# Kernel optimization log

Hardware: AMD Instinct MI355X
Metric: run time of the kernel (lower is better)

The kernel has to match this reference:

```python
import jax, jax.numpy as jnp
import numpy as np

N = 100000
E = 600000
H = 128
G = 64          # number of graphs
LN_EPS = 1e-5


def setup_inputs() -> dict:
    key = jax.random.key(0)
    ks = jax.random.split(key, 16)
    node = jax.random.normal(ks[0], (N, H), dtype=jnp.float32)
    edge_index = jax.random.randint(ks[1], (2, E), 0, N, dtype=jnp.int64)
    edge_attr = jax.random.normal(ks[2], (E, 1), dtype=jnp.float32)
    batch_ptr = jnp.sort(jax.random.randint(ks[3], (N,), 0, G, dtype=jnp.int64))
    s = 1.0 / np.sqrt(H)
    params = dict(
        eps=jnp.float32(0.0),  # GINConv train_eps=True, init 0
        W1=jax.random.uniform(ks[4], (H, H), jnp.float32, -s, s),
        b1=jnp.zeros((H,), jnp.float32),
        g1=jnp.ones((H,), jnp.float32), be1=jnp.zeros((H,), jnp.float32),
        W2=jax.random.uniform(ks[5], (H, H), jnp.float32, -s, s),
        b2=jnp.zeros((H,), jnp.float32),
        g2=jnp.ones((H,), jnp.float32), be2=jnp.zeros((H,), jnp.float32),
        W3=jax.random.uniform(ks[6], (H, H), jnp.float32, -s, s),
        b3=jnp.zeros((H,), jnp.float32),
        ln_w=jnp.ones((H,), jnp.float32), ln_b=jnp.zeros((H,), jnp.float32),
    )
    return dict(node=node, edge_index=edge_index, edge_attr=edge_attr,
                batch_ptr=batch_ptr, **params)


def _layernorm(x, g, b):
    mu = x.mean(-1, keepdims=True)
    var = ((x - mu) ** 2).mean(-1, keepdims=True)
    return (x - mu) * jax.lax.rsqrt(var + LN_EPS) * g + b


def _forward(node, edge_index, batch_ptr, eps, W1, b1, g1, be1, W2, b2, g2, be2,
             W3, b3, ln_w, ln_b):
    src, dst = edge_index[0], edge_index[1]
    # GIN sum aggregation: scatter-add neighbor features to targets
    agg = jax.ops.segment_sum(node[src], dst, num_segments=N)  # [N, H]
    h = (1.0 + eps) * node + agg
    # 3-layer MLP (PyG MLP: lin -> LayerNorm -> ReLU, final lin plain)
    h = jax.nn.relu(_layernorm(h @ W1 + b1, g1, be1))
    h = jax.nn.relu(_layernorm(h @ W2 + b2, g2, be2))
    h = h @ W3 + b3
    # PyG graph-mode LayerNorm: normalize over all nodes+features per graph
    cnt = jax.ops.segment_sum(jnp.ones((N,), h.dtype), batch_ptr, num_segments=G)
    norm = jnp.maximum(cnt * H, 1.0)                       # [G]
    mean = jax.ops.segment_sum(h.sum(-1), batch_ptr, num_segments=G) / norm
    hc = h - mean[batch_ptr][:, None]
    var = jax.ops.segment_sum((hc * hc).sum(-1), batch_ptr, num_segments=G) / norm
    out = hc * jax.lax.rsqrt(var + LN_EPS)[batch_ptr][:, None] * ln_w + ln_b
    return jax.nn.relu(out)


def reference(node, edge_index, edge_attr, batch_ptr, eps, W1, b1, g1, be1,
              W2, b2, g2, be2, W3, b3, ln_w, ln_b):
    del edge_attr  # accepted by GIN_Layer.forward but unused
    return _forward(node, edge_index, batch_ptr, eps, W1, b1, g1, be1,
                    W2, b2, g2, be2, W3, b3, ln_w, ln_b)
```

## Files before the change

### kernel.cpp

```cpp
#include <hip/hip_runtime.h>

#define N_NODES 100000
#define N_EDGES 600000
#define H 128
#define G_NUM 64
#define LN_EPS 1e-5f

#define WSTR 136

#define NTILES ((N_NODES + 63) / 64)

#define SCAN_CHUNK 1024
#define SCAN_NB ((N_NODES + SCAN_CHUNK - 1) / SCAN_CHUNK)
#define HIST_NB ((N_EDGES + 255) / 256)
#define CVT_NB ((N_NODES * H / 8 + 255) / 256)
#define FILL_NB ((N_EDGES + 255) / 256)
#define WT_NB ((3 * 16384 + 255) / 256)

#define SCR_MAX 272

#define WT_IOFF   900612
#define NBF_IOFF  925192
#define H0_BF_IOFF (NBF_IOFF + N_NODES * (H / 2))
#define NEEDED_MIN ((size_t)(NBF_IOFF + N_NODES * (H / 2)) * 4)
#define NEEDED_BF  ((size_t)(H0_BF_IOFF + N_NODES * (H / 2)) * 4)

typedef __attribute__((ext_vector_type(8))) short short8;
typedef __attribute__((ext_vector_type(4))) float floatx4;

__device__ __forceinline__ unsigned short f2bf(float x) {
    unsigned int u = __float_as_uint(x);
    u += 0x7fffu + ((u >> 16) & 1u);
    return (unsigned short)(u >> 16);
}

__global__ __launch_bounds__(256) void hist_cvt_kernel(
    const int* __restrict__ ei, int* __restrict__ deg,
    const float* __restrict__ node, unsigned int* __restrict__ node_bf)
{
    int gb = blockIdx.x;
    if (gb < HIST_NB) {
        int e = gb * 256 + threadIdx.x;
        if (e >= N_EDGES) return;
        atomicAdd(&deg[ei[N_EDGES + e]], 1);
    } else {
        int i = (gb - HIST_NB) * 256 + threadIdx.x;
        if (i >= N_NODES * H / 8) return;
        float4 a = ((const float4*)node)[i * 2];
        float4 b = ((const float4*)node)[i * 2 + 1];
        uint4 p;
        p.x = (unsigned)f2bf(a.x) | ((unsigned)f2bf(a.y) << 16);
        p.y = (unsigned)f2bf(a.z) | ((unsigned)f2bf(a.w) << 16);
        p.z = (unsigned)f2bf(b.x) | ((unsigned)f2bf(b.y) << 16);
        p.w = (unsigned)f2bf(b.z) | ((unsigned)f2bf(b.w) << 16);
        ((uint4*)node_bf)[i] = p;
    }
}

__global__ __launch_bounds__(256) void scan1_kernel(
    const int* __restrict__ deg, int* __restrict__ off,
    int* __restrict__ blksum)
{
    __shared__ int sA[256], sB[256];
    const int tid = threadIdx.x;
    const int base = blockIdx.x * SCAN_CHUNK + tid * 4;
    int v[4];
#pragma unroll
    for (int j = 0; j < 4; ++j) {
        int i = base + j;
        v[j] = (i < N_NODES) ? deg[i] : 0;
    }
    int tsum = v[0] + v[1] + v[2] + v[3];
    int* a = sA; int* b = sB;
    a[tid] = tsum;
    __syncthreads();
#pragma unroll
    for (int o = 1; o < 256; o <<= 1) {
        int t = a[tid] + ((tid >= o) ? a[tid - o] : 0);
        b[tid] = t;
        __syncthreads();
        int* tmp = a; a = b; b = tmp;
    }
    int run = a[tid] - tsum;
#pragma unroll
    for (int j = 0; j < 4; ++j) {
        int i = base + j;
        if (i < N_NODES) off[i] = run;
        run += v[j];
    }
    if (tid == 255) blksum[blockIdx.x] = a[255];
}

__global__ __launch_bounds__(256) void scan23_kernel(
    int* __restrict__ off, const int* __restrict__ blksum,
    int* __restrict__ cursor)
{
    __shared__ int sA[128], sB[128];
    const int tid = threadIdx.x;
    if (tid < 128) sA[tid] = (tid < SCAN_NB) ? blksum[tid] : 0;
    __syncthreads();
    int* a = sA; int* b = sB;
#pragma unroll
    for (int o = 1; o < 128; o <<= 1) {
        int t = 0;
        if (tid < 128) t = a[tid] + ((tid >= o) ? a[tid - o] : 0);
        __syncthreads();
        if (tid < 128) b[tid] = t;
        __syncthreads();
        int* tmp = a; a = b; b = tmp;
    }
    int excl = 0;
    if (tid < 128) excl = a[tid] - ((tid < SCAN_NB) ? blksum[tid] : 0);
    __syncthreads();
    if (tid < 128) sA[tid] = excl;
    __syncthreads();

    int i = blockIdx.x * 256 + tid;
    if (i < N_NODES) {
        int val = off[i] + sA[i >> 10];
        off[i] = val;
        cursor[i] = val;
    }
    if (i == 0) off[N_NODES] = N_EDGES;
}

__global__ __launch_bounds__(256) void fill_wt_kernel(
    const int* __restrict__ ei, int* __restrict__ cursor,
    int* __restrict__ csr,
    const float* __restrict__ W1, const float* __restrict__ W2,
    const float* __restrict__ W3, unsigned short* __restrict__ WT)
{
    int gb = blockIdx.x;
    if (gb < FILL_NB) {
        int e = gb * 256 + threadIdx.x;
        if (e >= N_EDGES) return;
        int dst = ei[N_EDGES + e];
        int pos = atomicAdd(&cursor[dst], 1);
        csr[pos] = ei[e];
    } else {
        int idx = (gb - FILL_NB) * 256 + threadIdx.x;
        if (idx >= 3 * 16384) return;
        int l = idx >> 14, r = idx & 16383;
        int frag = r >> 3, j = r & 7;
        int lane = frag & 63, ktnt = frag >> 6;
        int kt = ktnt & 3, nt = ktnt >> 2;
        int c = lane & 15, q = lane >> 4;
        int n = nt * 16 + c;
        int k = kt * 32 + q * 8 + j;
        const float* W = (l == 0) ? W1 : ((l == 1) ? W2 : W3);
        WT[l * 16384 + r] = f2bf(W[k * 128 + n]);
    }
}

template <bool NBF>
__global__ __launch_bounds__(256) void gather_kernel(
    const float* __restrict__ node, const unsigned int* __restrict__ nbf,
    const int* __restrict__ off, const int* __restrict__ csr,
    const float* __restrict__ epsp, unsigned int* __restrict__ h0)
{
    __shared__ int scr4[4][SCR_MAX];
    const int tid = threadIdx.x;
    const int w = tid >> 6, lane = tid & 63;
    const int n0 = blockIdx.x * 64 + w * 16;

    const float2* np2 = (const float2*)node;
    const float epsv = 1.0f + epsp[0];

    auto ld = [&](int n) -> float2 {
        if constexpr (NBF) {
            unsigned int u = nbf[(size_t)n * 64 + lane];
            return make_float2(__uint_as_float(u << 16),
                               __uint_as_float(u & 0xffff0000u));
        } else {
            return np2[(size_t)n * 64 + lane];
        }
    };

    int oidx = n0 + ((lane < 17) ? lane : 16);
    if (oidx > N_NODES) oidx = N_NODES;
    const int offl = off[oidx];
    const int e_begin = __shfl(offl, 0);
    const int e_end   = __shfl(offl, 16);
    const int cnt = e_end - e_begin;

    int* scr = scr4[w];

    if (cnt <= SCR_MAX) {
        for (int k = lane; k < cnt; k += 64) scr[k] = csr[e_begin + k];
        __threadfence_block();

#pragma unroll
        for (int g4 = 0; g4 < 4; ++g4) {
            int p[4], e[4];
#pragma unroll
            for (int j = 0; j < 4; ++j) {
                p[j] = __shfl(offl, g4 * 4 + j) - e_begin;
                e[j] = __shfl(offl, g4 * 4 + j + 1) - e_begin;
            }
            float2 acc[4];
#pragma unroll
            for (int j = 0; j < 4; ++j) {
                int n = n0 + g4 * 4 + j;
                if (n < N_NODES) {
                    float2 own = ld(n);
                    acc[j] = make_float2(epsv * own.x, epsv * own.y);
                } else {
                    acc[j] = make_float2(0.f, 0.f);
                }
            }
            bool a0[4], a1[4];
            float2 b0[4], b1[4];
#pragma unroll
            for (int j = 0; j < 4; ++j) {
                a0[j] = p[j] < e[j];
                b0[j] = make_float2(0.f, 0.f);
                if (a0[j]) {
                    int nb = __builtin_amdgcn_readfirstlane(scr[p[j]]);
                    b0[j] = ld(nb);
                }
            }
#pragma unroll
            for (int j = 0; j < 4; ++j) {
                a1[j] = (p[j] + 1) < e[j];
                b1[j] = make_float2(0.f, 0.f);
                if (a1[j]) {
                    int nb = __builtin_amdgcn_readfirstlane(scr[p[j] + 1]);
                    b1[j] = ld(nb);
                }
            }
            while (a0[0] || a0[1] || a0[2] || a0[3]) {
                float2 b2[4]; bool a2[4];
#pragma unroll
                for (int j = 0; j < 4; ++j) {
                    a2[j] = (p[j] + 2) < e[j];
                    b2[j] = make_float2(0.f, 0.f);
                    if (a2[j]) {
                        int nb = __builtin_amdgcn_readfirstlane(scr[p[j] + 2]);
                        b2[j] = ld(nb);
                    }
                }
#pragma unroll
                for (int j = 0; j < 4; ++j) {
                    if (a0[j]) {
                        acc[j].x += b0[j].x; acc[j].y += b0[j].y;
                        p[j] += 1;
                    }
                    a0[j] = a1[j]; b0[j] = b1[j];
                    a1[j] = a2[j]; b1[j] = b2[j];
                }
            }
#pragma unroll
            for (int j = 0; j < 4; ++j) {
                int n = n0 + g4 * 4 + j;
                if (n < N_NODES) {
                    unsigned int pk = (unsigned)f2bf(acc[j].x) |
                                      ((unsigned)f2bf(acc[j].y) << 16);
                    h0[(size_t)n * 64 + lane] = pk;
                }
            }
        }
    } else {
#pragma unroll
        for (int g4 = 0; g4 < 4; ++g4) {
            float2 acc[4];
#pragma unroll
            for (int j = 0; j < 4; ++j) {
                int n = n0 + g4 * 4 + j;
                if (n < N_NODES) {
                    float2 own = ld(n);
                    acc[j] = make_float2(epsv * own.x, epsv * own.y);
                } else {
                    acc[j] = make_float2(0.f, 0.f);
                }
            }
            for (int j = 0; j < 4; ++j) {
                int n = n0 + g4 * 4 + j;
                if (n >= N_NODES) continue;
                for (int t = off[n]; t < off[n + 1]; ++t) {
                    float2 v = ld(csr[t]);
                    acc[j].x += v.x; acc[j].y += v.y;
                }
            }
#pragma unroll
            for (int j = 0; j < 4; ++j) {
                int n = n0 + g4 * 4 + j;
                if (n < N_NODES) {
                    unsigned int pk = (unsigned)f2bf(acc[j].x) |
                                      ((unsigned)f2bf(acc[j].y) << 16);
                    h0[(size_t)n * 64 + lane] = pk;
                }
            }
        }
    }
}

__device__ __forceinline__ void gemm_frags(const unsigned short* hIn,
                                           const unsigned short* __restrict__ WTl,
                                           floatx4 acc[8], int w, int lane)
{
    const int c = lane & 15, q = lane >> 4;
#pragma unroll
    for (int nt = 0; nt < 8; ++nt) acc[nt] = (floatx4){0.f, 0.f, 0.f, 0.f};
#pragma unroll
    for (int kt = 0; kt < 4; ++kt) {
        short8 a = *(const short8*)&hIn[(w * 16 + c) * WSTR + kt * 32 + q * 8];
#pragma unroll
        for (int nt = 0; nt < 8; ++nt) {
            short8 b = *(const short8*)&WTl[(nt * 256 + kt * 64 + lane) * 8];
            acc[nt] = __builtin_amdgcn_mfma_f32_16x16x32_bf16(a, b, acc[nt], 0, 0, 0);
        }
    }
}

__device__ __forceinline__ void gemm_layer_ln(unsigned short* h,
                                              const unsigned short* __restrict__ WTl,
                                              const float* __restrict__ bias,
                                              const float* __restrict__ g,
                                              const float* __restrict__ be,
                                              int w, int lane)
{
    const int c = lane & 15, q = lane >> 4;
    floatx4 acc[8];
    gemm_frags(h, WTl, acc, w, lane);

    float sum[4] = {0.f, 0.f, 0.f, 0.f};
    float sq[4]  = {0.f, 0.f, 0.f, 0.f};
#pragma unroll
    for (int nt = 0; nt < 8; ++nt) {
        float bv = bias[nt * 16 + c];
#pragma unroll
        for (int i = 0; i < 4; ++i) {
            float vv = acc[nt][i] + bv;
            acc[nt][i] = vv;
            sum[i] += vv; sq[i] += vv * vv;
        }
    }
#pragma unroll
    for (int m = 1; m < 16; m <<= 1) {
#pragma unroll
        for (int i = 0; i < 4; ++i) {
            sum[i] += __shfl_xor(sum[i], m);
            sq[i]  += __shfl_xor(sq[i], m);
        }
    }
    float mu[4], rstd[4];
#pragma unroll
    for (int i = 0; i < 4; ++i) {
        mu[i]   = sum[i] * (1.0f / 128.0f);
        rstd[i] = rsqrtf(sq[i] * (1.0f / 128.0f) - mu[i] * mu[i] + LN_EPS);
    }
#pragma unroll
    for (int nt = 0; nt < 8; ++nt) {
        float gw = g[nt * 16 + c];
        float bw = be[nt * 16 + c];
#pragma unroll
        for (int i = 0; i < 4; ++i) {
            float val = fmaxf(0.f, (acc[nt][i] - mu[i]) * rstd[i] * gw + bw);
            h[(w * 16 + q * 4 + i) * WSTR + nt * 16 + c] = f2bf(val);
        }
    }
}

__global__ __launch_bounds__(256) void mlp_kernel(
    const unsigned int* __restrict__ h0,
    const unsigned short* __restrict__ WT,
    const float* __restrict__ b1, const float* __restrict__ g1,
    const float* __restrict__ be1,
    const float* __restrict__ b2, const float* __restrict__ g2,
    const float* __restrict__ be2,
    const float* __restrict__ b3, const int* __restrict__ batch,
    float* __restrict__ out, float* __restrict__ gstat)
{
    __shared__ unsigned short hA[64 * WSTR];
    __shared__ float prm[7 * 128];
    __shared__ float s_gsum[G_NUM], s_gsq[G_NUM], s_gcnt[G_NUM];

    const int tid = threadIdx.x;
    const int w = tid >> 6, lane = tid & 63;
    const int row0 = blockIdx.x * 64;

    if (tid < G_NUM) { s_gsum[tid] = 0.f; s_gsq[tid] = 0.f; s_gcnt[tid] = 0.f; }
    {
        const float* srcs[7] = {b1, g1, be1, b2, g2, be2, b3};
#pragma unroll
        for (int t = 0; t < 4; ++t) {
            int i = tid + t * 256;
            if (i < 7 * 128) prm[i] = srcs[i >> 7][i & 127];
        }
    }

    {
        const int r = tid >> 2;
        const int q4 = tid & 3;
        uint4* d = (uint4*)(((unsigned int*)hA) + r * (WSTR / 2) + q4 * 16);
        const int row = row0 + r;
        if (row < N_NODES) {
            const uint4* s = (const uint4*)&h0[(size_t)row * 64 + q4 * 16];
#pragma unroll
            for (int k = 0; k < 4; ++k) d[k] = s[k];
        } else {
            uint4 z = make_uint4(0, 0, 0, 0);
#pragma unroll
            for (int k = 0; k < 4; ++k) d[k] = z;
        }
    }
    __syncthreads();

    gemm_layer_ln(hA, WT,         &prm[0],   &prm[128], &prm[256], w, lane);
    gemm_layer_ln(hA, WT + 16384, &prm[384], &prm[512], &prm[640], w, lane);

    {
        const int c = lane & 15, q = lane >> 4;
        floatx4 acc3[8];
        gemm_frags(hA, WT + 32768, acc3, w, lane);
        float sum[4] = {0.f, 0.f, 0.f, 0.f};
        float sq[4]  = {0.f, 0.f, 0.f, 0.f};
#pragma unroll
        for (int nt = 0; nt < 8; ++nt) {
            float bv = prm[768 + nt * 16 + c];
#pragma unroll
            for (int i = 0; i < 4; ++i) {
                float vv = acc3[nt][i] + bv;
                size_t nrow = (size_t)row0 + w * 16 + q * 4 + i;
                if (nrow < N_NODES)
                    out[nrow * H + nt * 16 + c] = vv;
                sum[i] += vv; sq[i] += vv * vv;
            }
        }
#pragma unroll
        for (int m = 1; m < 16; m <<= 1) {
#pragma unroll
            for (int i = 0; i < 4; ++i) {
                sum[i] += __shfl_xor(sum[i], m);
                sq[i]  += __shfl_xor(sq[i], m);
            }
        }
        if (c == 0) {
#pragma unroll
            for (int i = 0; i < 4; ++i) {
                size_t nrow = (size_t)row0 + w * 16 + q * 4 + i;
                if (nrow < N_NODES) {
                    int g = batch[nrow];
                    atomicAdd(&s_gsum[g], sum[i]);
                    atomicAdd(&s_gsq[g], sq[i]);
                    atomicAdd(&s_gcnt[g], 1.0f);
                }
            }
        }
    }
    __syncthreads();
    if (tid < G_NUM && s_gcnt[tid] > 0.f) {
        unsafeAtomicAdd(&gstat[tid], s_gsum[tid]);
        unsafeAtomicAdd(&gstat[G_NUM + tid], s_gsq[tid]);
        unsafeAtomicAdd(&gstat[2 * G_NUM + tid], s_gcnt[tid]);
    }
}

__global__ __launch_bounds__(256) void final_ln_kernel(
    float* __restrict__ h3, const int* __restrict__ batch,
    const float* __restrict__ lnw, const float* __restrict__ lnb,
    const float* __restrict__ gstat)
{
    int idx4 = blockIdx.x * 256 + threadIdx.x;
    if (idx4 >= N_NODES * 32) return;
    int node = idx4 >> 5;
    int c4 = (idx4 & 31) * 4;
    int g = batch[node];
    float s   = gstat[g];
    float qq  = gstat[G_NUM + g];
    float cnt = gstat[2 * G_NUM + g];
    float norm = fmaxf(cnt * (float)H, 1.0f);
    float mean = s / norm;
    float var  = qq / norm - mean * mean;
    float inv  = rsqrtf(var + LN_EPS);
    float4 v = ((const float4*)h3)[idx4];
    float4 w = *(const float4*)&lnw[c4];
    float4 b = *(const float4*)&lnb[c4];
    v.x = fmaxf(0.f, (v.x - mean) * inv * w.x + b.x);
    v.y = fmaxf(0.f, (v.y - mean) * inv * w.y + b.y);
    v.z = fmaxf(0.f, (v.z - mean) * inv * w.z + b.z);
    v.w = fmaxf(0.f, (v.w - mean) * inv * w.w + b.w);
    ((float4*)h3)[idx4] = v;
}

extern "C" void kernel_launch(void* const* d_in, const int* in_sizes, int n_in,
                              void* d_out, int out_size, void* d_ws, size_t ws_size,
                              hipStream_t stream)
{
    const float* node  = (const float*)d_in[0];
    const int*   ei    = (const int*)d_in[1];
    const int*   batch = (const int*)d_in[3];
    const float* epsp  = (const float*)d_in[4];
    const float* W1    = (const float*)d_in[5];
    const float* b1    = (const float*)d_in[6];
    const float* g1    = (const float*)d_in[7];
    const float* be1   = (const float*)d_in[8];
    const float* W2    = (const float*)d_in[9];
    const float* b2    = (const float*)d_in[10];
    const float* g2    = (const float*)d_in[11];
    const float* be2   = (const float*)d_in[12];
    const float* W3    = (const float*)d_in[13];
    const float* b3    = (const float*)d_in[14];
    const float* lnw   = (const float*)d_in[15];
    const float* lnb   = (const float*)d_in[16];

    float* out = (float*)d_out;

    int* base = (int*)d_ws;
    float* gstat  = (float*)d_ws;
    int*   deg    = base + 512;
    int*   off    = deg + N_NODES;
    int*   cursor = off + N_NODES + 1;
    int*   csr    = cursor + N_NODES;
    int*   blksum = csr + N_EDGES;
    unsigned short* WT = (unsigned short*)(base + WT_IOFF);

    const bool use_bf = (ws_size >= NEEDED_BF);
    unsigned int* nbf = (unsigned int*)(base + NBF_IOFF);
    unsigned int* h0  = use_bf ? (unsigned int*)(base + H0_BF_IOFF)
                               : (unsigned int*)(base + NBF_IOFF);

    hipMemsetAsync(d_ws, 0, (512 + N_NODES) * sizeof(int), stream);

    hist_cvt_kernel<<<HIST_NB + (use_bf ? CVT_NB : 0), 256, 0, stream>>>(
        ei, deg, node, nbf);
    scan1_kernel<<<SCAN_NB, 256, 0, stream>>>(deg, off, blksum);
    scan23_kernel<<<(N_NODES + 255) / 256, 256, 0, stream>>>(off, blksum, cursor);
    fill_wt_kernel<<<FILL_NB + WT_NB, 256, 0, stream>>>(ei, cursor, csr,
                                                        W1, W2, W3, WT);

    if (use_bf)
        gather_kernel<true><<<NTILES, 256, 0, stream>>>(node, nbf, off, csr,
                                                        epsp, h0);
    else
        gather_kernel<false><<<NTILES, 256, 0, stream>>>(node, nbf, off, csr,
                                                         epsp, h0);

    mlp_kernel<<<NTILES, 256, 0, stream>>>(h0, WT, b1, g1, be1, b2, g2, be2,
                                           b3, batch, out, gstat);

    final_ln_kernel<<<(N_NODES * 32 + 255) / 256, 256, 0, stream>>>(
        out, batch, lnw, lnb, gstat);
}
```

Baseline: 344.5 us.

## Rewrite gather as block-wide edge-parallel LDS atomic accumulation

The gather kernel now processes a 64-node tile per block. Its edges are split evenly across the four waves, and each neighbor row is accumulated into a shared-memory fp32 tile with LDS atomics. This replaces the per-wave 16-node walk, which was serialized by node degree. The bf16 node copy is repacked so each 32-bit word holds columns c and c+64, matching the new load pattern. The change also adds an occupancy hint to the MLP kernel. It adds shared-memory atomics, more LDS use per block and extra barriers, which may lower occupancy.

```diff
diff --git a/kernel.cpp b/kernel.cpp
--- a/kernel.cpp
+++ b/kernel.cpp
@@ -17,12 +17,11 @@
 #define FILL_NB ((N_EDGES + 255) / 256)
 #define WT_NB ((3 * 16384 + 255) / 256)
 
-#define SCR_MAX 272
+#define EBUF 1536
 
 #define WT_IOFF   900612
 #define NBF_IOFF  925192
 #define H0_BF_IOFF (NBF_IOFF + N_NODES * (H / 2))
-#define NEEDED_MIN ((size_t)(NBF_IOFF + N_NODES * (H / 2)) * 4)
 #define NEEDED_BF  ((size_t)(H0_BF_IOFF + N_NODES * (H / 2)) * 4)
 
 typedef __attribute__((ext_vector_type(8))) short short8;
@@ -45,14 +44,16 @@
         atomicAdd(&deg[ei[N_EDGES + e]], 1);
     } else {
         int i = (gb - HIST_NB) * 256 + threadIdx.x;
-        if (i >= N_NODES * H / 8) return;
-        float4 a = ((const float4*)node)[i * 2];
-        float4 b = ((const float4*)node)[i * 2 + 1];
+        if (i >= N_NODES * 16) return;
+        int n = i >> 4;
+        int c0 = (i & 15) * 4;
+        const float4 a = *(const float4*)&node[(size_t)n * H + c0];
+        const float4 b = *(const float4*)&node[(size_t)n * H + 64 + c0];
         uint4 p;
-        p.x = (unsigned)f2bf(a.x) | ((unsigned)f2bf(a.y) << 16);
-        p.y = (unsigned)f2bf(a.z) | ((unsigned)f2bf(a.w) << 16);
-        p.z = (unsigned)f2bf(b.x) | ((unsigned)f2bf(b.y) << 16);
-        p.w = (unsigned)f2bf(b.z) | ((unsigned)f2bf(b.w) << 16);
+        p.x = (unsigned)f2bf(a.x) | ((unsigned)f2bf(b.x) << 16);
+        p.y = (unsigned)f2bf(a.y) | ((unsigned)f2bf(b.y) << 16);
+        p.z = (unsigned)f2bf(a.z) | ((unsigned)f2bf(b.z) << 16);
+        p.w = (unsigned)f2bf(a.w) | ((unsigned)f2bf(b.w) << 16);
         ((uint4*)node_bf)[i] = p;
     }
 }
@@ -158,138 +159,115 @@
     const int* __restrict__ off, const int* __restrict__ csr,
     const float* __restrict__ epsp, unsigned int* __restrict__ h0)
 {
-    __shared__ int scr4[4][SCR_MAX];
+    __shared__ float hacc[64][H];
+    __shared__ int   scr[EBUF];
+    __shared__ int   s_off[65];
+
     const int tid = threadIdx.x;
     const int w = tid >> 6, lane = tid & 63;
-    const int n0 = blockIdx.x * 64 + w * 16;
-
-    const float2* np2 = (const float2*)node;
+    const int row0 = blockIdx.x * 64;
     const float epsv = 1.0f + epsp[0];
 
-    auto ld = [&](int n) -> float2 {
-        if constexpr (NBF) {
-            unsigned int u = nbf[(size_t)n * 64 + lane];
-            return make_float2(__uint_as_float(u << 16),
-                               __uint_as_float(u & 0xffff0000u));
-        } else {
-            return np2[(size_t)n * 64 + lane];
-        }
-    };
-
-    int oidx = n0 + ((lane < 17) ? lane : 16);
-    if (oidx > N_NODES) oidx = N_NODES;
-    const int offl = off[oidx];
-    const int e_begin = __shfl(offl, 0);
-    const int e_end   = __shfl(offl, 16);
-    const int cnt = e_end - e_begin;
-
-    int* scr = scr4[w];
-
-    if (cnt <= SCR_MAX) {
-        for (int k = lane; k < cnt; k += 64) scr[k] = csr[e_begin + k];
-        __threadfence_block();
-
-#pragma unroll
-        for (int g4 = 0; g4 < 4; ++g4) {
-            int p[4], e[4];
-#pragma unroll
-            for (int j = 0; j < 4; ++j) {
-                p[j] = __shfl(offl, g4 * 4 + j) - e_begin;
-                e[j] = __shfl(offl, g4 * 4 + j + 1) - e_begin;
+    if (tid < 65) {
+        int r = row0 + tid;
+        s_off[tid] = off[(r > N_NODES) ? N_NODES : r];
+    }
+
+#pragma unroll
+    for (int i = 0; i < 16; ++i) {
+        int g = tid + 256 * i;
+        int row = g >> 6, c = g & 63;
+        int n = row0 + row;
+        float x0 = 0.f, x1 = 0.f;
+        if (n < N_NODES) {
+            if constexpr (NBF) {
+                unsigned int u = nbf[(size_t)n * 64 + c];
+                x0 = __uint_as_float(u << 16);
+                x1 = __uint_as_float(u & 0xffff0000u);
+            } else {
+                x0 = node[(size_t)n * H + c];
+                x1 = node[(size_t)n * H + 64 + c];
             }
-            float2 acc[4];
-#pragma unroll
-            for (int j = 0; j < 4; ++j) {
-                int n = n0 + g4 * 4 + j;
-                if (n < N_NODES) {
-                    float2 own = ld(n);
-                    acc[j] = make_float2(epsv * own.x, epsv * own.y);
-                } else {
-                    acc[j] = make_float2(0.f, 0.f);
+        }
+        hacc[row][c]      = epsv * x0;
+        hacc[row][64 + c] = epsv * x1;
+    }
+    __syncthreads();
+
+    const int e_begin = s_off[0];
+    const int cnt = s_off[64] - e_begin;
+
+    for (int cb = 0; cb < cnt; cb += EBUF) {
+        const int cwin = (cnt - cb < EBUF) ? (cnt - cb) : EBUF;
+        for (int k = tid; k < cwin; k += 256) scr[k] = csr[e_begin + cb + k];
+        __syncthreads();
+        {
+            const int r = tid >> 2, q = tid & 3;
+            int klo = s_off[r] - e_begin;     if (klo < cb) klo = cb;
+            int khi = s_off[r + 1] - e_begin; if (khi > cb + cwin) khi = cb + cwin;
+            for (int k = klo + q; k < khi; k += 4)
+                scr[k - cb] |= (r << 18);
+        }
+        __syncthreads();
+        const int cend = cb + cwin;
+        for (int base = cb + w * 8; base < cend; base += 32) {
+            const int m = (cend - base < 8) ? (cend - base) : 8;
+            if (m == 8) {
+                int nbv[8], rv[8];
+#pragma unroll
+                for (int j = 0; j < 8; ++j) {
+                    int pk = __builtin_amdgcn_readfirstlane(scr[base - cb + j]);
+                    nbv[j] = pk & 0x3FFFF;
+                    rv[j] = pk >> 18;
+                }
+                float vx[8], vy[8];
+#pragma unroll
+                for (int j = 0; j < 8; ++j) {
+                    if constexpr (NBF) {
+                        unsigned int u = nbf[(size_t)nbv[j] * 64 + lane];
+                        vx[j] = __uint_as_float(u << 16);
+                        vy[j] = __uint_as_float(u & 0xffff0000u);
+                    } else {
+                        vx[j] = node[(size_t)nbv[j] * H + lane];
+                        vy[j] = node[(size_t)nbv[j] * H + 64 + lane];
+                    }
+                }
+#pragma unroll
+                for (int j = 0; j < 8; ++j) {
+                    atomicAdd(&hacc[rv[j]][lane], vx[j]);
+                    atomicAdd(&hacc[rv[j]][64 + lane], vy[j]);
+                }
+            } else {
+                for (int j = 0; j < m; ++j) {
+                    int pk = __builtin_amdgcn_readfirstlane(scr[base - cb + j]);
+                    int nb = pk & 0x3FFFF;
+                    int r  = pk >> 18;
+                    float x0, x1;
+                    if constexpr (NBF) {
+                        unsigned int u = nbf[(size_t)nb * 64 + lane];
+                        x0 = __uint_as_float(u << 16);
+                        x1 = __uint_as_float(u & 0xffff0000u);
+                    } else {
+                        x0 = node[(size_t)nb * H + lane];
+                        x1 = node[(size_t)nb * H + 64 + lane];
+                    }
+                    atomicAdd(&hacc[r][lane], x0);
+                    atomicAdd(&hacc[r][64 + lane], x1);
                 }
             }
-            bool a0[4], a1[4];
-            float2 b0[4], b1[4];
-#pragma unroll
-            for (int j = 0; j < 4; ++j) {
-                a0[j] = p[j] < e[j];
-                b0[j] = make_float2(0.f, 0.f);
-                if (a0[j]) {
-                    int nb = __builtin_amdgcn_readfirstlane(scr[p[j]]);
-                    b0[j] = ld(nb);
-                }
-            }
-#pragma unroll
-            for (int j = 0; j < 4; ++j) {
-                a1[j] = (p[j] + 1) < e[j];
-                b1[j] = make_float2(0.f, 0.f);
-                if (a1[j]) {
-                    int nb = __builtin_amdgcn_readfirstlane(scr[p[j] + 1]);
-                    b1[j] = ld(nb);
-                }
-            }
-            while (a0[0] || a0[1] || a0[2] || a0[3]) {
-                float2 b2[4]; bool a2[4];
-#pragma unroll
-                for (int j = 0; j < 4; ++j) {
-                    a2[j] = (p[j] + 2) < e[j];
-                    b2[j] = make_float2(0.f, 0.f);
-                    if (a2[j]) {
-                        int nb = __builtin_amdgcn_readfirstlane(scr[p[j] + 2]);
-                        b2[j] = ld(nb);
-                    }
-                }
-#pragma unroll
-                for (int j = 0; j < 4; ++j) {
-                    if (a0[j]) {
-                        acc[j].x += b0[j].x; acc[j].y += b0[j].y;
-                        p[j] += 1;
-                    }
-                    a0[j] = a1[j]; b0[j] = b1[j];
-                    a1[j] = a2[j]; b1[j] = b2[j];
-                }
-            }
-#pragma unroll
-            for (int j = 0; j < 4; ++j) {
-                int n = n0 + g4 * 4 + j;
-                if (n < N_NODES) {
-                    unsigned int pk = (unsigned)f2bf(acc[j].x) |
-                                      ((unsigned)f2bf(acc[j].y) << 16);
-                    h0[(size_t)n * 64 + lane] = pk;
-                }
-            }
-        }
-    } else {
-#pragma unroll
-        for (int g4 = 0; g4 < 4; ++g4) {
-            float2 acc[4];
-#pragma unroll
-            for (int j = 0; j < 4; ++j) {
-                int n = n0 + g4 * 4 + j;
-                if (n < N_NODES) {
-                    float2 own = ld(n);
-                    acc[j] = make_float2(epsv * own.x, epsv * own.y);
-                } else {
-                    acc[j] = make_float2(0.f, 0.f);
-                }
-            }
-            for (int j = 0; j < 4; ++j) {
-                int n = n0 + g4 * 4 + j;
-                if (n >= N_NODES) continue;
-                for (int t = off[n]; t < off[n + 1]; ++t) {
-                    float2 v = ld(csr[t]);
-                    acc[j].x += v.x; acc[j].y += v.y;
-                }
-            }
-#pragma unroll
-            for (int j = 0; j < 4; ++j) {
-                int n = n0 + g4 * 4 + j;
-                if (n < N_NODES) {
-                    unsigned int pk = (unsigned)f2bf(acc[j].x) |
-                                      ((unsigned)f2bf(acc[j].y) << 16);
-                    h0[(size_t)n * 64 + lane] = pk;
-                }
-            }
+        }
+        __syncthreads();
+    }
+
+#pragma unroll
+    for (int i = 0; i < 16; ++i) {
+        int g = tid + 256 * i;
+        int row = g >> 6, c = g & 63;
+        int n = row0 + row;
+        if (n < N_NODES) {
+            unsigned int pk = (unsigned)f2bf(hacc[row][2 * c]) |
+                              ((unsigned)f2bf(hacc[row][2 * c + 1]) << 16);
+            h0[(size_t)n * 64 + c] = pk;
         }
     }
 }
@@ -361,7 +339,7 @@
     }
 }
 
-__global__ __launch_bounds__(256) void mlp_kernel(
+__global__ __launch_bounds__(256, 4) void mlp_kernel(
     const unsigned int* __restrict__ h0,
     const unsigned short* __restrict__ WT,
     const float* __restrict__ b1, const float* __restrict__ g1,
```

Measured after the change: 698.6 us. 2.03x slower.

## Restructure gather to per-node 8-wide batched neighbor loads; bound MLP occupancy

Applied to the files above, without the earlier changes.

The gather kernel used to interleave four nodes with a depth-3 software pipeline over their neighbor lists. It now processes one node at a time and issues up to eight neighbor row loads at once before accumulating them. The oversized-segment fallback is folded into the same loop by reading indices from global memory instead of LDS. This aims to expose more memory-level parallelism per wave for the typical degree of about six, at the cost of serializing nodes. Separately, the MLP kernel gets a launch-bounds occupancy hint of 4 blocks, which may limit its register use.

```diff
diff --git a/kernel.cpp b/kernel.cpp
--- a/kernel.cpp
+++ b/kernel.cpp
@@ -22,7 +22,6 @@
 #define WT_IOFF   900612
 #define NBF_IOFF  925192
 #define H0_BF_IOFF (NBF_IOFF + N_NODES * (H / 2))
-#define NEEDED_MIN ((size_t)(NBF_IOFF + N_NODES * (H / 2)) * 4)
 #define NEEDED_BF  ((size_t)(H0_BF_IOFF + N_NODES * (H / 2)) * 4)
 
 typedef __attribute__((ext_vector_type(8))) short short8;
@@ -162,19 +161,9 @@
     const int tid = threadIdx.x;
     const int w = tid >> 6, lane = tid & 63;
     const int n0 = blockIdx.x * 64 + w * 16;
+    const float epsv = 1.0f + epsp[0];
 
     const float2* np2 = (const float2*)node;
-    const float epsv = 1.0f + epsp[0];
-
-    auto ld = [&](int n) -> float2 {
-        if constexpr (NBF) {
-            unsigned int u = nbf[(size_t)n * 64 + lane];
-            return make_float2(__uint_as_float(u << 16),
-                               __uint_as_float(u & 0xffff0000u));
-        } else {
-            return np2[(size_t)n * 64 + lane];
-        }
-    };
 
     int oidx = n0 + ((lane < 17) ? lane : 16);
     if (oidx > N_NODES) oidx = N_NODES;
@@ -184,113 +173,67 @@
     const int cnt = e_end - e_begin;
 
     int* scr = scr4[w];
-
-    if (cnt <= SCR_MAX) {
+    const bool use_scr = (cnt <= SCR_MAX);
+    if (use_scr) {
         for (int k = lane; k < cnt; k += 64) scr[k] = csr[e_begin + k];
         __threadfence_block();
-
-#pragma unroll
-        for (int g4 = 0; g4 < 4; ++g4) {
-            int p[4], e[4];
-#pragma unroll
-            for (int j = 0; j < 4; ++j) {
-                p[j] = __shfl(offl, g4 * 4 + j) - e_begin;
-                e[j] = __shfl(offl, g4 * 4 + j + 1) - e_begin;
-            }
-            float2 acc[4];
-#pragma unroll
-            for (int j = 0; j < 4; ++j) {
-                int n = n0 + g4 * 4 + j;
-                if (n < N_NODES) {
-                    float2 own = ld(n);
-                    acc[j] = make_float2(epsv * own.x, epsv * own.y);
-                } else {
-                    acc[j] = make_float2(0.f, 0.f);
+    }
+
+    for (int i = 0; i < 16; ++i) {
+        int n = n0 + i;
+        if (n >= N_NODES) break;
+        const int kb = __shfl(offl, i) - e_begin;
+        const int ke = __shfl(offl, i + 1) - e_begin;
+
+        float a0, a1;
+        if constexpr (NBF) {
+            unsigned uo = nbf[(size_t)n * 64 + lane];
+            a0 = epsv * __uint_as_float(uo << 16);
+            a1 = epsv * __uint_as_float(uo & 0xffff0000u);
+        } else {
+            float2 own = np2[(size_t)n * 64 + lane];
+            a0 = epsv * own.x;
+            a1 = epsv * own.y;
+        }
+
+        for (int k = kb; k < ke; k += 8) {
+            const int m = ke - k;
+            if constexpr (NBF) {
+                unsigned uu[8];
+#pragma unroll
+                for (int j = 0; j < 8; ++j) {
+                    if (j < m) {
+                        int nb = __builtin_amdgcn_readfirstlane(
+                            use_scr ? scr[k + j] : csr[e_begin + k + j]);
+                        uu[j] = nbf[(size_t)nb * 64 + lane];
+                    }
+                }
+#pragma unroll
+                for (int j = 0; j < 8; ++j) {
+                    if (j < m) {
+                        a0 += __uint_as_float(uu[j] << 16);
+                        a1 += __uint_as_float(uu[j] & 0xffff0000u);
+                    }
+                }
+            } else {
+                float2 vv[8];
+#pragma unroll
+                for (int j = 0; j < 8; ++j) {
+                    if (j < m) {
+                        int nb = __builtin_amdgcn_readfirstlane(
+                            use_scr ? scr[k + j] : csr[e_begin + k + j]);
+                        vv[j] = np2[(size_t)nb * 64 + lane];
+                    }
+                }
+#pragma unroll
+                for (int j = 0; j < 8; ++j) {
+                    if (j < m) { a0 += vv[j].x; a1 += vv[j].y; }
                 }
             }
-            bool a0[4], a1[4];
-            float2 b0[4], b1[4];
-#pragma unroll
-            for (int j = 0; j < 4; ++j) {
-                a0[j] = p[j] < e[j];
-                b0[j] = make_float2(0.f, 0.f);
-                if (a0[j]) {
-                    int nb = __builtin_amdgcn_readfirstlane(scr[p[j]]);
-                    b0[j] = ld(nb);
-                }
-            }
-#pragma unroll
-            for (int j = 0; j < 4; ++j) {
-                a1[j] = (p[j] + 1) < e[j];
-                b1[j] = make_float2(0.f, 0.f);
-                if (a1[j]) {
-                    int nb = __builtin_amdgcn_readfirstlane(scr[p[j] + 1]);
-                    b1[j] = ld(nb);
-                }
-            }
-            while (a0[0] || a0[1] || a0[2] || a0[3]) {
-                float2 b2[4]; bool a2[4];
-#pragma unroll
-                for (int j = 0; j < 4; ++j) {
-                    a2[j] = (p[j] + 2) < e[j];
-                    b2[j] = make_float2(0.f, 0.f);
-                    if (a2[j]) {
-                        int nb = __builtin_amdgcn_readfirstlane(scr[p[j] + 2]);
-                        b2[j] = ld(nb);
-                    }
-                }
-#pragma unroll
-                for (int j = 0; j < 4; ++j) {
-                    if (a0[j]) {
-                        acc[j].x += b0[j].x; acc[j].y += b0[j].y;
-                        p[j] += 1;
-                    }
-                    a0[j] = a1[j]; b0[j] = b1[j];
-                    a1[j] = a2[j]; b1[j] = b2[j];
-                }
-            }
-#pragma unroll
-            for (int j = 0; j < 4; ++j) {
-                int n = n0 + g4 * 4 + j;
-                if (n < N_NODES) {
-                    unsigned int pk = (unsigned)f2bf(acc[j].x) |
-                                      ((unsigned)f2bf(acc[j].y) << 16);
-                    h0[(size_t)n * 64 + lane] = pk;
-                }
-            }
-        }
-    } else {
-#pragma unroll
-        for (int g4 = 0; g4 < 4; ++g4) {
-            float2 acc[4];
-#pragma unroll
-            for (int j = 0; j < 4; ++j) {
-                int n = n0 + g4 * 4 + j;
-                if (n < N_NODES) {
-                    float2 own = ld(n);
-                    acc[j] = make_float2(epsv * own.x, epsv * own.y);
-                } else {
-                    acc[j] = make_float2(0.f, 0.f);
-                }
-            }
-            for (int j = 0; j < 4; ++j) {
-                int n = n0 + g4 * 4 + j;
-                if (n >= N_NODES) continue;
-                for (int t = off[n]; t < off[n + 1]; ++t) {
-                    float2 v = ld(csr[t]);
-                    acc[j].x += v.x; acc[j].y += v.y;
-                }
-            }
-#pragma unroll
-            for (int j = 0; j < 4; ++j) {
-                int n = n0 + g4 * 4 + j;
-                if (n < N_NODES) {
-                    unsigned int pk = (unsigned)f2bf(acc[j].x) |
-                                      ((unsigned)f2bf(acc[j].y) << 16);
-                    h0[(size_t)n * 64 + lane] = pk;
-                }
-            }
-        }
+        }
+
+        unsigned pk = (unsigned)f2bf(a0) | ((unsigned)f2bf(a1) << 16);
+        h0[(size_t)n * 64 + lane] = pk;
     }
 }
 
@@ -361,7 +304,7 @@
     }
 }
 
-__global__ __launch_bounds__(256) void mlp_kernel(
+__global__ __launch_bounds__(256, 4) void mlp_kernel(
     const unsigned int* __restrict__ h0,
     const unsigned short* __restrict__ WT,
     const float* __restrict__ b1, const float* __restrict__ g1,
```

Measured after the change: 304.1 us. -11.7%, faster.
